# Performance work log

Hardware: AMD Instinct MI355X
Metric: run time of the kernel (lower is better)

Reference implementation:

```python
import jax, jax.numpy as jnp
import numpy as np

EPS = 1e-6
T = 8            # max_recursion_depth
STACK = 16       # stack_size
K = 1024         # n_symbols
CC = 0.25        # commitment_cost
ETH_W = 0.005    # ethical_weight
PONDER = 1e-4    # ponder_penalty
B, DIM, V = 1024, 512, 32000


def _clin(Wr, Wi, zr, zi):
    # complex linear: (Wr + i Wi)(zr + i zi), nn.Linear convention x @ W.T
    return zr @ Wr.T - zi @ Wi.T, zi @ Wr.T + zr @ Wi.T


def _cnorm(scale, shift, zr, zi):
    mag = jnp.sqrt(zr * zr + zi * zi) + EPS
    mean = mag.mean(-1, keepdims=True)
    var = mag.var(-1, keepdims=True, ddof=1)  # torch.var unbiased=True
    nm = (mag - mean) / jnp.sqrt(var + EPS) * scale + shift
    ph = jnp.arctan2(zi, zr)
    return nm * jnp.cos(ph), nm * jnp.sin(ph)


def _modrelu(b, zr, zi):
    n = jnp.sqrt(zr * zr + zi * zi) + EPS
    s = jax.nn.relu(n + b) / n
    return zr * s, zi * s


def setup_inputs() -> dict:
    key = jax.random.key(0)
    ks = jax.random.split(key, 24)
    g = lambda k, sh, s=0.02: (jax.random.normal(k, sh, jnp.float32) * s)
    xav = lambda k, sh: jax.random.uniform(k, sh, jnp.float32, -1, 1) * np.sqrt(6.0 / (sh[0] + sh[1]))
    return {
        'input_ids': jax.random.randint(ks[0], (B, 1), 0, V),
        'emb_mag': g(ks[1], (V, DIM), 1.0),
        'emb_phase': g(ks[2], (V, DIM), 1.0),
        'lin_r': xav(ks[3], (DIM, DIM)), 'lin_i': xav(ks[4], (DIM, DIM)),
        'norm_scale': jnp.ones((DIM,), jnp.float32), 'norm_shift': jnp.zeros((DIM,), jnp.float32),
        'mod_bias': jnp.zeros((DIM,), jnp.float32),
        'halt_W': g(ks[5], (1, 2 * DIM)), 'halt_b': jnp.full((1,), -2.0, jnp.float32),
        'ctrl_W': g(ks[6], (3, 2 * DIM)), 'ctrl_b': jnp.zeros((3,), jnp.float32),
        'q_r': xav(ks[7], (DIM, DIM)), 'q_i': xav(ks[8], (DIM, DIM)),
        'k_r': xav(ks[9], (DIM, DIM)), 'k_i': xav(ks[10], (DIM, DIM)),
        'v_r': xav(ks[11], (DIM, DIM)), 'v_i': xav(ks[12], (DIM, DIM)),
        'codebook': jax.random.normal(ks[13], (K, 2 * DIM), jnp.float32),
        'adjacency': jnp.zeros((K, K), jnp.float32),
        'dec_W': g(ks[14], (V, 2 * DIM)), 'dec_b': jnp.zeros((V,), jnp.float32),
    }


def reference(input_ids, emb_mag, emb_phase, lin_r, lin_i, norm_scale, norm_shift, mod_bias,
              halt_W, halt_b, ctrl_W, ctrl_b, q_r, q_i, k_r, k_i, v_r, v_i,
              codebook, adjacency, dec_W, dec_b):
    dim = emb_mag.shape[1]
    b = input_ids.shape[0]
    idx = input_ids[:, 0]
    r, th = emb_mag[idx], emb_phase[idx]
    zr, zi = r * jnp.cos(th), r * jnp.sin(th)  # [B, dim] complex embedding

    mem = jnp.zeros((b, STACK, 2 * dim), zr.dtype)
    ptr = jnp.zeros((b, STACK), zr.dtype).at[:, 0].set(1.0)
    remain = jnp.ones((b, 1), zr.dtype)
    zwr = jnp.zeros_like(zr); zwi = jnp.zeros_like(zi)
    ponder = jnp.float32(0.0); vq_tot = jnp.float32(0.0)
    eth_tot = jnp.float32(0.0); prev = None
    scale = dim ** -0.5

    for step in range(T):
        # AdaptiveRecursiveCell: linear -> norm -> modrelu -> attention
        pr, pi = _clin(lin_r, lin_i, zr, zi)
        pr, pi = _cnorm(norm_scale, norm_shift, pr, pi)
        pr, pi = _modrelu(mod_bias, pr, pi)
        qr, qi = _clin(q_r, q_i, pr, pi)
        kr, ki = _clin(k_r, k_i, pr, pi)
        vr, vi = _clin(v_r, v_i, pr, pi)
        qf = jnp.concatenate([qr, qi], -1)
        kf = jnp.concatenate([kr, ki], -1)
        A = jax.nn.softmax(qf @ kf.T * scale, -1)  # [B, B] cross-batch attention
        pr, pi = A @ vr, A @ vi
        zf = jnp.concatenate([pr, pi], -1)  # [B, 2dim]
        halt = jax.nn.sigmoid(zf @ halt_W.T + halt_b)        # [B, 1]
        ctrl = jax.nn.softmax(zf @ ctrl_W.T + ctrl_b, -1)    # [B, 3]

        # DifferentiableStack
        push, pop, noop = ctrl[:, :1], ctrl[:, 1:2], ctrl[:, 2:3]
        ptr_up = jnp.roll(ptr, 1, axis=1)
        ptr_dn = jnp.roll(ptr, -1, axis=1)
        nptr = push * ptr_up + pop * ptr_dn + noop * ptr
        nptr = nptr / (nptr.sum(1, keepdims=True) + EPS)
        wm = push * ptr_up  # [B, STACK]
        mem = wm[:, :, None] * zf[:, None, :] + mem * (1.0 - wm[:, :, None])
        read = (mem * nptr[:, :, None]).sum(1)  # [B, 2dim]
        ptr = nptr
        cr = pr + read[:, :dim]; ci = pi + read[:, dim:]

        # GraphMemoryVQ (batched path: graph bias branch is a no-op)
        cf = jnp.concatenate([cr, ci], -1)
        d = ((cf * cf).sum(-1, keepdims=True) + (codebook * codebook).sum(-1)
             - 2.0 * cf @ codebook.T)  # [B, K]
        sym = jnp.argmin(d, -1)
        zq = codebook[sym]
        vq_tot = vq_tot + jnp.mean((zq - jax.lax.stop_gradient(cf)) ** 2) \
                 + CC * jnp.mean((jax.lax.stop_gradient(zq) - cf) ** 2)
        zq = cf + jax.lax.stop_gradient(zq - cf)  # straight-through
        sr, si = zq[:, :dim], zq[:, dim:]

        # EthicalConstraint: cross_entropy(adjacency[prev], curr)
        if prev is not None:
            row = adjacency[prev]  # [B, K]
            eth = jnp.mean(jax.nn.logsumexp(row, -1)
                           - jnp.take_along_axis(row, sym[:, None], 1)[:, 0])
            eth_tot = eth_tot + eth
        prev = sym

        # ACT weighting
        w = remain if step == T - 1 else halt * remain
        zwr = zwr + w * sr; zwi = zwi + w * si
        remain = remain * (1.0 - halt)
        ponder = ponder + remain.mean()
        zr, zi = sr, si

    logits = jnp.concatenate([zwr, zwi], -1) @ dec_W.T + dec_b  # [B, V]
    aux_loss = vq_tot + ETH_W * eth_tot + PONDER * ponder
    return logits, aux_loss
```

## Files before the change

kernel.cpp:

```cpp
#include <hip/hip_runtime.h>
#include <math.h>

#define NB 1024
#define ND 512
#define ND2 1024
#define NSTEPS 8
#define NSTACK 16
#define NK 1024
#define NV 32000
#define FEPS 1e-6f
#define ATT_SCALE 0.044194173824159216f

typedef _Float16 f16;
typedef f16 f16x8 __attribute__((ext_vector_type(8)));
typedef f16 f16x4 __attribute__((ext_vector_type(4)));
typedef float f32x4 __attribute__((ext_vector_type(4)));

__device__ __forceinline__ int swz(int row, int chunk) {
    return row * 32 + ((chunk ^ ((row >> 1) & 3)) * 8);
}

__device__ __forceinline__ void gl16(const f16* g, f16* l) {
    __builtin_amdgcn_global_load_lds(
        (const __attribute__((address_space(1))) void*)g,
        (__attribute__((address_space(3))) void*)l, 16, 0, 0);
}

__device__ __forceinline__ float blk_sum(float v, float* red) {
    int t = threadIdx.x;
    red[t] = v; __syncthreads();
    for (int s = 128; s > 0; s >>= 1) {
        if (t < s) red[t] += red[t + s];
        __syncthreads();
    }
    float r = red[0]; __syncthreads();
    return r;
}

__device__ __forceinline__ float blk_max(float v, float* red) {
    int t = threadIdx.x;
    red[t] = v; __syncthreads();
    for (int s = 128; s > 0; s >>= 1) {
        if (t < s) red[t] = fmaxf(red[t], red[t + s]);
        __syncthreads();
    }
    float r = red[0]; __syncthreads();
    return r;
}

__device__ __forceinline__ void split_write(float v, f16* oh, f16* ol, size_t idx) {
    f16 h = (f16)v;
    oh[idx] = h;
    ol[idx] = (f16)((v - (float)h) * 1024.f);
}

__global__ __launch_bounds__(256)
void k_init(float* ptrb, float* remainb, float* scal) {
    int i = blockIdx.x * 256 + threadIdx.x;
    if (i < NB) {
        remainb[i] = 1.f;
        for (int s = 0; s < NSTACK; ++s) ptrb[i * NSTACK + s] = (s == 0) ? 1.f : 0.f;
    }
    if (i < 8) scal[i] = 0.f;
}

__global__ __launch_bounds__(256)
void k_embed(const int* __restrict__ ids, const float* __restrict__ mag,
             const float* __restrict__ ph, f16* __restrict__ zh, f16* __restrict__ zl) {
    int b = blockIdx.x;
    int id = ids[b];
    for (int d = threadIdx.x; d < ND; d += 256) {
        float m = mag[(size_t)id * ND + d];
        float p = ph[(size_t)id * ND + d];
        split_write(m * cosf(p), zh, zl, (size_t)b * ND2 + d);
        split_write(m * sinf(p), zh, zl, (size_t)b * ND2 + ND + d);
    }
}

__global__ __launch_bounds__(256)
void k_cbnorm(const float* __restrict__ cb, float* __restrict__ cbn) {
    __shared__ float red[256];
    int k = blockIdx.x;
    float s = 0.f;
    for (int c = threadIdx.x; c < ND2; c += 256) {
        float v = cb[(size_t)k * ND2 + c];
        s += v * v;
    }
    float tot = blk_sum(s, red);
    if (threadIdx.x == 0) cbn[k] = tot;
}

__global__ __launch_bounds__(256)
void k_lse(const float* __restrict__ adj, float* __restrict__ lse) {
    __shared__ float red[256];
    int k = blockIdx.x, t = threadIdx.x;
    float lm = -INFINITY;
    for (int c = t; c < NK; c += 256) lm = fmaxf(lm, adj[(size_t)k * NK + c]);
    float mxa = blk_max(lm, red);
    float le = 0.f;
    for (int c = t; c < NK; c += 256) le += expf(adj[(size_t)k * NK + c] - mxa);
    float se = blk_sum(le, red);
    if (t == 0) lse[k] = mxa + logf(se);
}

__global__ __launch_bounds__(256)
void k_buildW(const float* __restrict__ Wr, const float* __restrict__ Wi,
              f16* __restrict__ oh, f16* __restrict__ ol, int transp) {
    int idx = blockIdx.x * 256 + threadIdx.x;
    int n = idx >> 10, k = idx & 1023;
    int r = transp ? k : n, c = transp ? n : k;
    float v;
    if (r < 512) v = (c < 512) ? Wr[r * 512 + c] : -Wi[r * 512 + (c - 512)];
    else { int r2 = r - 512; v = (c < 512) ? Wi[r2 * 512 + c] : Wr[r2 * 512 + (c - 512)]; }
    split_write(v, oh, ol, idx);
}

__global__ __launch_bounds__(256)
void k_splitcb(const float* __restrict__ in, f16* __restrict__ oh, f16* __restrict__ ol) {
    int idx = blockIdx.x * 256 + threadIdx.x;
    split_write(in[idx], oh, ol, idx);
}

__global__ __launch_bounds__(256)
void k_split_h(const float* __restrict__ in, f16* __restrict__ oh, size_t n) {
    size_t i = (size_t)blockIdx.x * 256 + threadIdx.x;
    size_t st = (size_t)gridDim.x * 256;
    for (; i < n; i += st) oh[i] = (f16)in[i];
}

__global__ __launch_bounds__(256)
void k_split1(const float* __restrict__ in, f16* __restrict__ oh, f16* __restrict__ ol) {
    int idx = blockIdx.x * 256 + threadIdx.x;
    split_write(in[idx], oh, ol, idx);
}

template<int EPI>
__global__ __launch_bounds__(512, 4)
void k_sgemm5(const f16* __restrict__ Ah, const f16* __restrict__ Al,
              const f16* __restrict__ Bh, const f16* __restrict__ Bl,
              float* __restrict__ Cf,
              f16* __restrict__ qh, f16* __restrict__ ql,
              f16* __restrict__ vTh, f16* __restrict__ vTl,
              int N, int K, float alpha) {
    __shared__ f16 lds[2][2][4][64 * 32];
    const int tid = threadIdx.x;
    const int g = tid >> 8;
    const int gt = tid & 255;
    const int srow = gt >> 2, scb = gt & 3;
    const int soff = swz(srow, scb);
    const int lane = tid & 63;
    const int q = (tid >> 6) & 3;
    const int qr = (q >> 1) * 32, qc = (q & 1) * 32;
    const int fr = lane & 15, cbk = lane >> 4;
    const int m0 = blockIdx.y * 64, n0 = blockIdx.x * 64;
    const int kbase = g * (K >> 1);
    const int iters = K >> 6;

    const f16* pA  = Ah + (size_t)(m0 + srow) * K + kbase + scb * 8;
    const f16* pAl_ = Al + (size_t)(m0 + srow) * K + kbase + scb * 8;
    const f16* pB  = Bh + (size_t)(n0 + srow) * K + kbase + scb * 8;
    const f16* pBl_ = Bl + (size_t)(n0 + srow) * K + kbase + scb * 8;

    f32x4 z4 = {0.f, 0.f, 0.f, 0.f};
    f32x4 acc0[2][2] = {{z4, z4}, {z4, z4}};
    f32x4 acc1[2][2] = {{z4, z4}, {z4, z4}};

    f16x8 rA  = *(const f16x8*)pA;
    f16x8 rAl = *(const f16x8*)pAl_;
    f16x8 rB  = *(const f16x8*)pB;
    f16x8 rBl = *(const f16x8*)pBl_;
    *(f16x8*)&lds[0][g][0][soff] = rA;
    *(f16x8*)&lds[0][g][1][soff] = rAl;
    *(f16x8*)&lds[0][g][2][soff] = rB;
    *(f16x8*)&lds[0][g][3][soff] = rBl;
    if (iters > 1) {
        rA  = *(const f16x8*)(pA + 32);
        rAl = *(const f16x8*)(pAl_ + 32);
        rB  = *(const f16x8*)(pB + 32);
        rBl = *(const f16x8*)(pBl_ + 32);
    }
    __syncthreads();

    for (int it = 0; it < iters; ++it) {
        const int cur = it & 1;
        f16x8 ah[2], al[2], bh[2], bl[2];
        #pragma unroll
        for (int i = 0; i < 2; ++i) {
            int ra = qr + i * 16 + fr;
            int oa = swz(ra, cbk);
            ah[i] = *(const f16x8*)&lds[cur][g][0][oa];
            al[i] = *(const f16x8*)&lds[cur][g][1][oa];
            int rb = qc + i * 16 + fr;
            int ob = swz(rb, cbk);
            bh[i] = *(const f16x8*)&lds[cur][g][2][ob];
            bl[i] = *(const f16x8*)&lds[cur][g][3][ob];
        }
        if (it + 1 < iters) {
            *(f16x8*)&lds[cur ^ 1][g][0][soff] = rA;
            *(f16x8*)&lds[cur ^ 1][g][1][soff] = rAl;
            *(f16x8*)&lds[cur ^ 1][g][2][soff] = rB;
            *(f16x8*)&lds[cur ^ 1][g][3][soff] = rBl;
            if (it + 2 < iters) {
                int ko = (it + 2) * 32;
                rA  = *(const f16x8*)(pA + ko);
                rAl = *(const f16x8*)(pAl_ + ko);
                rB  = *(const f16x8*)(pB + ko);
                rBl = *(const f16x8*)(pBl_ + ko);
            }
        }
        #pragma unroll
        for (int i = 0; i < 2; ++i)
            #pragma unroll
            for (int j = 0; j < 2; ++j) {
                acc0[i][j] = __builtin_amdgcn_mfma_f32_16x16x32_f16(ah[i], bh[j], acc0[i][j], 0, 0, 0);
                acc1[i][j] = __builtin_amdgcn_mfma_f32_16x16x32_f16(ah[i], bl[j], acc1[i][j], 0, 0, 0);
                acc1[i][j] = __builtin_amdgcn_mfma_f32_16x16x32_f16(al[i], bh[j], acc1[i][j], 0, 0, 0);
            }
        __syncthreads();
    }

    float val[2][2][4];
    #pragma unroll
    for (int i = 0; i < 2; ++i)
        #pragma unroll
        for (int j = 0; j < 2; ++j)
            #pragma unroll
            for (int jj = 0; jj < 4; ++jj)
                val[i][j][jj] = acc0[i][j][jj] + acc1[i][j][jj] * 9.765625e-4f;

    float* red = (float*)&lds[0][0][0][0];
    if (g == 1) {
        #pragma unroll
        for (int i = 0; i < 2; ++i)
            #pragma unroll
            for (int j = 0; j < 2; ++j) {
                int r = i * 16 + (lane >> 4) * 4, c = j * 16 + (lane & 15);
                #pragma unroll
                for (int jj = 0; jj < 4; ++jj)
                    red[q * 1056 + (r + jj) * 33 + c] = val[i][j][jj];
            }
    }
    __syncthreads();
    if (g == 0) {
        #pragma unroll
        for (int i = 0; i < 2; ++i)
            #pragma unroll
            for (int j = 0; j < 2; ++j) {
                int r = i * 16 + (lane >> 4) * 4, c = j * 16 + (lane & 15);
                #pragma unroll
                for (int jj = 0; jj < 4; ++jj)
                    val[i][j][jj] += red[q * 1056 + (r + jj) * 33 + c];
                int orow = m0 + qr + r;
                int ocol = n0 + qc + c;
                if constexpr (EPI == 0) {
                    #pragma unroll
                    for (int jj = 0; jj < 4; ++jj)
                        Cf[(size_t)(orow + jj) * N + ocol] = alpha * val[i][j][jj];
                } else {
                    int sec = ocol >> 10, lc = ocol & 1023;
                    if (sec == 0) {
                        #pragma unroll
                        for (int jj = 0; jj < 4; ++jj)
                            split_write(val[i][j][jj], qh, ql, (size_t)(orow + jj) * ND2 + lc);
                    } else {
                        f16x4 th, tl;
                        #pragma unroll
                        for (int jj = 0; jj < 4; ++jj) {
                            float v = val[i][j][jj];
                            f16 h = (f16)v;
                            th[jj] = h;
                            tl[jj] = (f16)((v - (float)h) * 1024.f);
                        }
                        *(f16x4*)&vTh[(size_t)lc * ND2 + orow] = th;
                        *(f16x4*)&vTl[(size_t)lc * ND2 + orow] = tl;
                    }
                }
            }
    }
}

__global__ __launch_bounds__(512, 4)
void k_dgemm6(const f16* __restrict__ A, const f16* __restrict__ B,
              float* __restrict__ C, const float* __restrict__ bias) {
    __shared__ f16 sA[2][256 * 32];
    __shared__ f16 sB[2][128 * 32];
    const int bid = blockIdx.x;
    const int l2 = (bid & 7) * 125 + (bid >> 3);
    const int m0 = (l2 & 3) * 256;
    const int n0 = (l2 >> 2) * 128;
    const int tid = threadIdx.x;
    const int lane = tid & 63, w = tid >> 6;
    const int wr = (w >> 1) * 64, wc = (w & 1) * 64;
    const int fr = lane & 15, cbk = lane >> 4;
    const int K = ND2;
    const int srow = lane >> 2, pch = lane & 3;

    f32x4 z4 = {0.f, 0.f, 0.f, 0.f};
    f32x4 acc[4][4];
    #pragma unroll
    for (int i = 0; i < 4; ++i)
        #pragma unroll
        for (int j = 0; j < 4; ++j) acc[i][j] = z4;

    auto STAGE = [&](int itn, int nbuf) {
        int ko = itn * 32;
        #pragma unroll
        for (int c = 0; c < 3; ++c) {
            int m = w * 3 + c;
            if (m < 16) {
                int row = m * 16 + srow;
                int chunk = (pch ^ ((row >> 1) & 3)) * 8;
                gl16(A + (size_t)(m0 + row) * K + ko + chunk, (f16*)&sA[nbuf][m * 512]);
            } else {
                int mm = m - 16;
                int row = mm * 16 + srow;
                int chunk = (pch ^ ((row >> 1) & 3)) * 8;
                gl16(B + (size_t)(n0 + row) * K + ko + chunk, (f16*)&sB[nbuf][mm * 512]);
            }
        }
    };

    STAGE(0, 0);
    __syncthreads();

    for (int it = 0; it < 32; ++it) {
        const int cur = it & 1;
        if (it + 1 < 32) STAGE(it + 1, cur ^ 1);
        f16x8 a[4], b[4];
        #pragma unroll
        for (int i = 0; i < 4; ++i) {
            int rra = wr + i * 16 + fr;
            a[i] = *(const f16x8*)&sA[cur][swz(rra, cbk)];
        }
        #pragma unroll
        for (int j = 0; j < 4; ++j) {
            int rrb = wc + j * 16 + fr;
            b[j] = *(const f16x8*)&sB[cur][swz(rrb, cbk)];
        }
        #pragma unroll
        for (int i = 0; i < 4; ++i)
            #pragma unroll
            for (int j = 0; j < 4; ++j)
                acc[i][j] = __builtin_amdgcn_mfma_f32_16x16x32_f16(a[i], b[j], acc[i][j], 0, 0, 0);
        __syncthreads();
    }
    #pragma unroll
    for (int i = 0; i < 4; ++i)
        #pragma unroll
        for (int j = 0; j < 4; ++j) {
            int orow = m0 + wr + i * 16 + (lane >> 4) * 4;
            int ocol = n0 + wc + j * 16 + (lane & 15);
            float bv = bias[ocol];
            #pragma unroll
            for (int jj = 0; jj < 4; ++jj)
                C[(size_t)(orow + jj) * NV + ocol] = acc[i][j][jj] + bv;
        }
}

__global__ __launch_bounds__(256)
void k_cnorm(const float* __restrict__ p, const float* __restrict__ CW1,
             const int* __restrict__ sym,
             f16* __restrict__ ph, f16* __restrict__ pl,
             const float* __restrict__ scale, const float* __restrict__ shift,
             const float* __restrict__ mbias) {
    __shared__ float red[256];
    int b = blockIdx.x, t = threadIdx.x;
    const float* row = sym ? (CW1 + (size_t)sym[b] * ND2) : (p + (size_t)b * ND2);
    float xr[2], xi[2], hv[2];
    float lsum = 0.f;
    #pragma unroll
    for (int l = 0; l < 2; ++l) {
        int d = t + l * 256;
        float a = row[d], c = row[ND + d];
        xr[l] = a; xi[l] = c;
        float h = sqrtf(a * a + c * c);
        hv[l] = h;
        lsum += h + FEPS;
    }
    float mean = blk_sum(lsum, red) * (1.f / ND);
    float lvar = 0.f;
    #pragma unroll
    for (int l = 0; l < 2; ++l) {
        float dv = (hv[l] + FEPS) - mean;
        lvar += dv * dv;
    }
    float var = blk_sum(lvar, red) * (1.f / (ND - 1));
    float istd = 1.f / sqrtf(var + FEPS);
    #pragma unroll
    for (int l = 0; l < 2; ++l) {
        int d = t + l * 256;
        float nm = ((hv[l] + FEPS) - mean) * istd * scale[d] + shift[d];
        float cc, ss;
        if (hv[l] > 0.f) { cc = xr[l] / hv[l]; ss = xi[l] / hv[l]; }
        else             { cc = 1.f; ss = 0.f; }
        float vr_ = nm * cc, vi_ = nm * ss;
        float n = sqrtf(vr_ * vr_ + vi_ * vi_) + FEPS;
        float aarg = n + mbias[d];
        float sg = (aarg > 0.f ? aarg : 0.f) / n;
        split_write(vr_ * sg, ph, pl, (size_t)b * ND2 + d);
        split_write(vi_ * sg, ph, pl, (size_t)b * ND2 + ND + d);
    }
}

__global__ __launch_bounds__(256)
void k_softmax2(const float* __restrict__ SS, const int* __restrict__ sym,
                f16* __restrict__ Ah, f16* __restrict__ Al) {
    __shared__ float red[256];
    __shared__ int syms[NB];
    int row = blockIdx.x, t = threadIdx.x;
    for (int i = t; i < NB; i += 256) syms[i] = sym[i];
    __syncthreads();
    const float* Srow = SS + (size_t)syms[row] * NK;
    float v[4];
    float lm = -INFINITY;
    #pragma unroll
    for (int l = 0; l < 4; ++l) {
        v[l] = ATT_SCALE * Srow[syms[t + l * 256]];
        lm = fmaxf(lm, v[l]);
    }
    float mx = blk_max(lm, red);
    float ls = 0.f;
    #pragma unroll
    for (int l = 0; l < 4; ++l) { v[l] = expf(v[l] - mx); ls += v[l]; }
    float tot = blk_sum(ls, red);
    float inv = 1024.f / tot;
    #pragma unroll
    for (int l = 0; l < 4; ++l)
        split_write(v[l] * inv, Ah, Al, (size_t)row * NB + t + l * 256);
}

__global__ __launch_bounds__(256)
void k_gatherVT(const f16* __restrict__ VTh, const f16* __restrict__ VTl,
                const int* __restrict__ sym,
                f16* __restrict__ vTh, f16* __restrict__ vTl) {
    __shared__ int syms[NB];
    int n = blockIdx.x, t = threadIdx.x;
    for (int i = t; i < NB; i += 256) syms[i] = sym[i];
    __syncthreads();
    const f16* rh = VTh + (size_t)n * NK;
    const f16* rl = VTl + (size_t)n * NK;
    for (int b = t; b < NB; b += 256) {
        int s = syms[b];
        vTh[(size_t)n * NB + b] = rh[s];
        vTl[(size_t)n * NB + b] = rl[s];
    }
}

__global__ __launch_bounds__(256)
void k_softmax(const float* __restrict__ S, f16* __restrict__ Ah, f16* __restrict__ Al) {
    __shared__ float red[256];
    int row = blockIdx.x, t = threadIdx.x;
    float v[4];
    float lm = -INFINITY;
    #pragma unroll
    for (int l = 0; l < 4; ++l) {
        v[l] = S[(size_t)row * NB + t + l * 256];
        lm = fmaxf(lm, v[l]);
    }
    float mx = blk_max(lm, red);
    float ls = 0.f;
    #pragma unroll
    for (int l = 0; l < 4; ++l) { v[l] = expf(v[l] - mx); ls += v[l]; }
    float tot = blk_sum(ls, red);
    float inv = 1024.f / tot;
    #pragma unroll
    for (int l = 0; l < 4; ++l)
        split_write(v[l] * inv, Ah, Al, (size_t)row * NB + t + l * 256);
}

__global__ __launch_bounds__(256)
void k_stack2(const float* __restrict__ zfh, int step,
              const float* __restrict__ hW, const float* __restrict__ hB,
              const float* __restrict__ cW, const float* __restrict__ cB,
              float* __restrict__ ptrb, float* __restrict__ Ptab,
              float* __restrict__ haltb, float* __restrict__ cfn,
              f16* __restrict__ cfh, f16* __restrict__ cfl) {
    __shared__ float zfs[ND2];
    __shared__ float red[256];
    __shared__ float pt[NSTACK], npv[NSTACK], wmv[NSTACK];
    __shared__ float coef[NSTEPS];
    __shared__ float snorm;
    int b = blockIdx.x, t = threadIdx.x;
    const float* zf = zfh + (size_t)step * NB * ND2 + (size_t)b * ND2;
    for (int c = t; c < ND2; c += 256) zfs[c] = zf[c];
    __syncthreads();
    float dh = 0, d0 = 0, d1 = 0, d2 = 0;
    for (int c = t; c < ND2; c += 256) {
        float z = zfs[c];
        dh += z * hW[c];
        d0 += z * cW[c];
        d1 += z * cW[ND2 + c];
        d2 += z * cW[2 * ND2 + c];
    }
    dh = blk_sum(dh, red);
    d0 = blk_sum(d0, red);
    d1 = blk_sum(d1, red);
    d2 = blk_sum(d2, red);
    float h = 1.f / (1.f + expf(-(dh + hB[0])));
    float l0 = d0 + cB[0], l1 = d1 + cB[1], l2 = d2 + cB[2];
    float mx = fmaxf(l0, fmaxf(l1, l2));
    float e0 = expf(l0 - mx), e1 = expf(l1 - mx), e2 = expf(l2 - mx);
    float es = e0 + e1 + e2;
    float push = e0 / es, pop = e1 / es, noop = e2 / es;
    if (t < NSTACK) pt[t] = ptrb[b * NSTACK + t];
    __syncthreads();
    if (t < NSTACK) {
        float up = pt[(t + NSTACK - 1) & 15];
        float dn = pt[(t + 1) & 15];
        npv[t] = push * up + pop * dn + noop * pt[t];
        wmv[t] = push * up;
    }
    __syncthreads();
    if (t == 0) {
        float s = 0.f;
        for (int j = 0; j < NSTACK; ++j) s += npv[j];
        snorm = 1.f / (s + FEPS);
    }
    __syncthreads();
    if (t < NSTACK) {
        npv[t] *= snorm;
        ptrb[b * NSTACK + t] = npv[t];
        float om = 1.f - wmv[t];
        for (int u = 0; u < step; ++u)
            Ptab[((size_t)b * NSTEPS + u) * NSTACK + t] *= om;
        Ptab[((size_t)b * NSTEPS + step) * NSTACK + t] = wmv[t];
    }
    __syncthreads();
    if (t <= step) {
        float s = 0.f;
        #pragma unroll
        for (int j = 0; j < NSTACK; ++j)
            s += npv[j] * Ptab[((size_t)b * NSTEPS + t) * NSTACK + j];
        coef[t] = s;
    }
    __syncthreads();
    float lq = 0.f;
    for (int c = t; c < ND2; c += 256) {
        float rd = coef[step] * zfs[c];
        for (int u = 0; u < step; ++u)
            rd += coef[u] * zfh[(size_t)u * NB * ND2 + (size_t)b * ND2 + c];
        float v = zfs[c] + rd;
        split_write(v, cfh, cfl, (size_t)b * ND2 + c);
        lq += v * v;
    }
    float q = blk_sum(lq, red);
    if (t == 0) { cfn[b] = q; haltb[b] = h; }
}

__global__ __launch_bounds__(256)
void k_vqstep(const float* __restrict__ G, const float* __restrict__ cb,
              const float* __restrict__ cbn, const float* __restrict__ cfn,
              const float* __restrict__ adj, const float* __restrict__ lse,
              const float* __restrict__ haltb,
              float* __restrict__ remainb, float* __restrict__ zw,
              f16* __restrict__ zwh, f16* __restrict__ zwl,
              int* __restrict__ prev, float* __restrict__ scal,
              int step, int islast) {
    __shared__ float sval[256];
    __shared__ int sidx[256];
    int b = blockIdx.x, t = threadIdx.x;
    float bv = INFINITY; int bi = NK;
    for (int k = t; k < NK; k += 256) {
        float v = cbn[k] - 2.f * G[(size_t)b * NK + k];
        if (v < bv) { bv = v; bi = k; }
    }
    sval[t] = bv; sidx[t] = bi;
    __syncthreads();
    for (int s = 128; s > 0; s >>= 1) {
        if (t < s) {
            float ov = sval[t + s]; int oi = sidx[t + s];
            if (ov < sval[t] || (ov == sval[t] && oi < sidx[t])) { sval[t] = ov; sidx[t] = oi; }
        }
        __syncthreads();
    }
    int sym = sidx[0];
    float sdt = sval[0] + cfn[b];
    float contrib = 0.f;
    if (step > 0) {
        int pv = prev[b];
        contrib = lse[pv] - adj[(size_t)pv * NK + sym];
    }
    float hb = haltb[b];
    float rm = remainb[b];
    float w = islast ? rm : hb * rm;
    for (int c = t; c < ND2; c += 256) {
        size_t idx = (size_t)b * ND2 + c;
        float nv = zw[idx] + w * cb[(size_t)sym * ND2 + c];
        if (islast) split_write(nv, zwh, zwl, idx);
        else zw[idx] = nv;
    }
    if (t == 0) {
        float nrm = rm * (1.f - hb);
        remainb[b] = nrm;
        atomicAdd(&scal[0], sdt);
        if (step > 0) atomicAdd(&scal[1], contrib);
        atomicAdd(&scal[2], nrm);
        prev[b] = sym;
    }
}

__global__ void k_aux(const float* __restrict__ scal, float* __restrict__ out) {
    out[0] = 1.25f * scal[0] / (1024.f * 1024.f)
           + 0.005f * (scal[1] / 1024.f)
           + 0.0001f * (scal[2] / 1024.f);
}

extern "C" void kernel_launch(void* const* d_in, const int* in_sizes, int n_in,
                              void* d_out, int out_size, void* d_ws, size_t ws_size,
                              hipStream_t stream) {
    const int*   input_ids  = (const int*)  d_in[0];
    const float* emb_mag    = (const float*)d_in[1];
    const float* emb_phase  = (const float*)d_in[2];
    const float* lin_r      = (const float*)d_in[3];
    const float* lin_i      = (const float*)d_in[4];
    const float* norm_scale = (const float*)d_in[5];
    const float* norm_shift = (const float*)d_in[6];
    const float* mod_bias   = (const float*)d_in[7];
    const float* halt_W     = (const float*)d_in[8];
    const float* halt_b     = (const float*)d_in[9];
    const float* ctrl_W     = (const float*)d_in[10];
    const float* ctrl_b     = (const float*)d_in[11];
    const float* q_r        = (const float*)d_in[12];
    const float* q_i        = (const float*)d_in[13];
    const float* k_r        = (const float*)d_in[14];
    const float* k_i        = (const float*)d_in[15];
    const float* v_r        = (const float*)d_in[16];
    const float* v_i        = (const float*)d_in[17];
    const float* codebook   = (const float*)d_in[18];
    const float* adjacency  = (const float*)d_in[19];
    const float* dec_W      = (const float*)d_in[20];
    const float* dec_b      = (const float*)d_in[21];
    float* out = (float*)d_out;

    float* fb = (float*)d_ws;
    size_t o = 0;
    auto af = [&](size_t n) { float* p = fb + o; o += n; return p; };
    float* scr      = af((size_t)NB * ND2);
    float* SS       = af((size_t)NK * NK);
    float* zfh      = af((size_t)NSTEPS * NB * ND2);
    float* CW1      = af((size_t)NK * ND2);
    float* zw       = af((size_t)NB * ND2);
    float* Ptab     = af((size_t)NB * NSTEPS * NSTACK);
    float* ptrb     = af((size_t)NB * NSTACK);
    float* haltb    = af(NB);
    float* remainb  = af(NB);
    float* cbn      = af(NK);
    float* cfn      = af(NB);
    float* lse      = af(NK);
    int*   prev     = (int*)af(NB);
    float* scal     = af(8);

    f16* hbuf = (f16*)(fb + o);
    size_t ho = 0;
    auto ah = [&](size_t n) { f16* q = hbuf + ho; ho += n; return q; };
    f16* z_h   = ah((size_t)NB * ND2);
    f16* z_l   = ah((size_t)NB * ND2);
    f16* p_h   = ah((size_t)NB * ND2);
    f16* p_l   = ah((size_t)NB * ND2);
    f16* t_h   = ah((size_t)NB * ND2);
    f16* t_l   = ah((size_t)NB * ND2);
    f16* vT_h  = ah((size_t)NB * ND2);
    f16* vT_l  = ah((size_t)NB * ND2);
    f16* VTt_h = ah((size_t)ND2 * NK);
    f16* VTt_l = ah((size_t)ND2 * NK);
    f16* Pn_h  = ah((size_t)NK * ND2);
    f16* Pn_l  = ah((size_t)NK * ND2);
    f16* A_h   = ah((size_t)NB * NB);
    f16* A_l   = ah((size_t)NB * NB);
    f16* cf_h  = ah((size_t)NB * ND2);
    f16* cf_l  = ah((size_t)NB * ND2);
    f16* zw_h  = ah((size_t)NB * ND2);
    f16* zw_l  = ah((size_t)NB * ND2);
    f16* W1_h  = ah((size_t)ND2 * ND2);
    f16* W1_l  = ah((size_t)ND2 * ND2);
    f16* WqT_h = ah((size_t)ND2 * ND2);
    f16* WqT_l = ah((size_t)ND2 * ND2);
    f16* WkT_h = ah((size_t)ND2 * ND2);
    f16* WkT_l = ah((size_t)ND2 * ND2);
    f16* Bc_h  = ah((size_t)2 * ND2 * ND2);
    f16* Bc_l  = ah((size_t)2 * ND2 * ND2);
    f16* cb_h  = ah((size_t)NK * ND2);
    f16* cb_l  = ah((size_t)NK * ND2);
    f16* dW_h  = ah((size_t)NV * ND2);

    hipMemsetAsync(zw, 0, (size_t)NB * ND2 * sizeof(float), stream);
    k_init<<<4, 256, 0, stream>>>(ptrb, remainb, scal);
    k_embed<<<NB, 256, 0, stream>>>(input_ids, emb_mag, emb_phase, z_h, z_l);
    k_cbnorm<<<NK, 256, 0, stream>>>(codebook, cbn);
    k_lse<<<NK, 256, 0, stream>>>(adjacency, lse);
    k_buildW<<<(ND2 * ND2) / 256, 256, 0, stream>>>(lin_r, lin_i, W1_h, W1_l, 0);
    k_buildW<<<(ND2 * ND2) / 256, 256, 0, stream>>>(q_r, q_i, WqT_h, WqT_l, 1);
    k_buildW<<<(ND2 * ND2) / 256, 256, 0, stream>>>(k_r, k_i, WkT_h, WkT_l, 1);
    k_buildW<<<(ND2 * ND2) / 256, 256, 0, stream>>>(v_r, v_i,
        Bc_h + (size_t)ND2 * ND2, Bc_l + (size_t)ND2 * ND2, 0);
    k_splitcb<<<(NK * ND2) / 256, 256, 0, stream>>>(codebook, cb_h, cb_l);
    k_split_h<<<2048, 256, 0, stream>>>(dec_W, dW_h, (size_t)NV * ND2);
    k_sgemm5<0><<<dim3(16, 16), 512, 0, stream>>>(WkT_h, WkT_l, WqT_h, WqT_l, scr,
        nullptr, nullptr, nullptr, nullptr, ND2, ND2, 1.f);
    k_split1<<<(ND2 * ND2) / 256, 256, 0, stream>>>(scr, Bc_h, Bc_l);
    k_sgemm5<0><<<dim3(16, 16), 512, 0, stream>>>(cb_h, cb_l, W1_h, W1_l, CW1,
        nullptr, nullptr, nullptr, nullptr, ND2, ND2, 1.f);
    k_cnorm<<<NK, 256, 0, stream>>>(CW1, nullptr, nullptr, Pn_h, Pn_l,
                                    norm_scale, norm_shift, mod_bias);
    k_sgemm5<2><<<dim3(32, 16), 512, 0, stream>>>(Pn_h, Pn_l, Bc_h, Bc_l, nullptr,
        t_h, t_l, VTt_h, VTt_l, 2 * ND2, ND2, 1.f);
    k_sgemm5<0><<<dim3(16, 16), 512, 0, stream>>>(t_h, t_l, Pn_h, Pn_l, SS,
        nullptr, nullptr, nullptr, nullptr, NK, ND2, 1.f);

    for (int step = 0; step < NSTEPS; ++step) {
        if (step == 0) {
            k_sgemm5<0><<<dim3(16, 16), 512, 0, stream>>>(z_h, z_l, W1_h, W1_l, scr,
                nullptr, nullptr, nullptr, nullptr, ND2, ND2, 1.f);
            k_cnorm<<<NB, 256, 0, stream>>>(scr, nullptr, nullptr, p_h, p_l,
                                            norm_scale, norm_shift, mod_bias);
            k_sgemm5<2><<<dim3(32, 16), 512, 0, stream>>>(p_h, p_l, Bc_h, Bc_l, nullptr,
                t_h, t_l, vT_h, vT_l, 2 * ND2, ND2, 1.f);
            k_sgemm5<0><<<dim3(16, 16), 512, 0, stream>>>(t_h, t_l, p_h, p_l, scr,
                nullptr, nullptr, nullptr, nullptr, NB, ND2, ATT_SCALE);
            k_softmax<<<NB, 256, 0, stream>>>(scr, A_h, A_l);
        } else {
            k_softmax2<<<NB, 256, 0, stream>>>(SS, prev, A_h, A_l);
            k_gatherVT<<<ND2, 256, 0, stream>>>(VTt_h, VTt_l, prev, vT_h, vT_l);
        }
        k_sgemm5<0><<<dim3(16, 16), 512, 0, stream>>>(A_h, A_l, vT_h, vT_l,
            zfh + (size_t)step * NB * ND2,
            nullptr, nullptr, nullptr, nullptr, ND2, NB, 9.765625e-4f);
        k_stack2<<<NB, 256, 0, stream>>>(zfh, step, halt_W, halt_b, ctrl_W, ctrl_b,
                                         ptrb, Ptab, haltb, cfn, cf_h, cf_l);
        k_sgemm5<0><<<dim3(16, 16), 512, 0, stream>>>(cf_h, cf_l, cb_h, cb_l, scr,
            nullptr, nullptr, nullptr, nullptr, NK, ND2, 1.f);
        k_vqstep<<<NB, 256, 0, stream>>>(scr, codebook, cbn, cfn, adjacency, lse, haltb, remainb,
                                         zw, zw_h, zw_l, prev, scal, step, step == NSTEPS - 1 ? 1 : 0);
    }
    k_dgemm6<<<1000, 512, 0, stream>>>(zw_h, dW_h, out, dec_b);
    k_aux<<<1, 1, 0, stream>>>(scal, out + (size_t)NB * NV);
}
```

Before: 1.184 ms.

## Fuse VQ argmin into codebook GEMM epilogue and merge softmax/gather kernels

Measured after the change: 1.198 ms. No clear change (+1.3%).

```diff
diff --git a/kernel.cpp b/kernel.cpp
--- a/kernel.cpp
+++ b/kernel.cpp
@@ -15,6 +15,7 @@
 typedef f16 f16x8 __attribute__((ext_vector_type(8)));
 typedef f16 f16x4 __attribute__((ext_vector_type(4)));
 typedef float f32x4 __attribute__((ext_vector_type(4)));
+typedef unsigned long long u64;
 
 __device__ __forceinline__ int swz(int row, int chunk) {
     return row * 32 + ((chunk ^ ((row >> 1) & 3)) * 8);
@@ -24,6 +25,21 @@
     __builtin_amdgcn_global_load_lds(
         (const __attribute__((address_space(1))) void*)g,
         (__attribute__((address_space(3))) void*)l, 16, 0, 0);
+}
+
+__device__ __forceinline__ u64 fkey(float v, int idx) {
+    unsigned int ub = __float_as_uint(v);
+    unsigned int ord = (ub & 0x80000000u) ? ~ub : (ub | 0x80000000u);
+    return ((u64)ord << 32) | (unsigned int)idx;
+}
+
+__device__ __forceinline__ void amin_lds(u64* a, u64 k) {
+    u64 old = *a;
+    while (k < old) {
+        u64 prev = atomicCAS(a, old, k);
+        if (prev == old) break;
+        old = prev;
+    }
 }
 
 __device__ __forceinline__ float blk_sum(float v, float* red) {
@@ -55,10 +71,11 @@
 }
 
 __global__ __launch_bounds__(256)
-void k_init(float* ptrb, float* remainb, float* scal) {
+void k_init(float* ptrb, float* remainb, float* scal, u64* amin) {
     int i = blockIdx.x * 256 + threadIdx.x;
     if (i < NB) {
         remainb[i] = 1.f;
+        amin[i] = ~0ULL;
         for (int s = 0; s < NSTACK; ++s) ptrb[i * NSTACK + s] = (s == 0) ? 1.f : 0.f;
     }
     if (i < 8) scal[i] = 0.f;
@@ -141,8 +158,10 @@
               float* __restrict__ Cf,
               f16* __restrict__ qh, f16* __restrict__ ql,
               f16* __restrict__ vTh, f16* __restrict__ vTl,
-              int N, int K, float alpha) {
+              int N, int K, float alpha,
+              const float* __restrict__ cbnv, u64* __restrict__ amin) {
     __shared__ f16 lds[2][2][4][64 * 32];
+    __shared__ u64 aml[64];
     const int tid = threadIdx.x;
     const int g = tid >> 8;
     const int gt = tid & 255;
@@ -239,6 +258,9 @@
                 for (int jj = 0; jj < 4; ++jj)
                     red[q * 1056 + (r + jj) * 33 + c] = val[i][j][jj];
             }
+        if constexpr (EPI == 3) {
+            if (gt < 64) aml[gt] = ~0ULL;
+        }
     }
     __syncthreads();
     if (g == 0) {
@@ -256,7 +278,7 @@
                     #pragma unroll
                     for (int jj = 0; jj < 4; ++jj)
                         Cf[(size_t)(orow + jj) * N + ocol] = alpha * val[i][j][jj];
-                } else {
+                } else if constexpr (EPI == 2) {
                     int sec = ocol >> 10, lc = ocol & 1023;
                     if (sec == 0) {
                         #pragma unroll
@@ -274,8 +296,19 @@
                         *(f16x4*)&vTh[(size_t)lc * ND2 + orow] = th;
                         *(f16x4*)&vTl[(size_t)lc * ND2 + orow] = tl;
                     }
+                } else {
+                    float cbv = cbnv[ocol];
+                    #pragma unroll
+                    for (int jj = 0; jj < 4; ++jj) {
+                        float v = cbv - 2.f * val[i][j][jj];
+                        amin_lds(&aml[qr + r + jj], fkey(v, ocol));
+                    }
                 }
             }
+    }
+    if constexpr (EPI == 3) {
+        __syncthreads();
+        if (tid < 64) atomicMin(&amin[m0 + tid], aml[tid]);
     }
 }
 
@@ -403,46 +436,43 @@
 }
 
 __global__ __launch_bounds__(256)
-void k_softmax2(const float* __restrict__ SS, const int* __restrict__ sym,
-                f16* __restrict__ Ah, f16* __restrict__ Al) {
+void k_attprep(const float* __restrict__ SS, const int* __restrict__ sym,
+               const f16* __restrict__ VTh, const f16* __restrict__ VTl,
+               f16* __restrict__ Ah, f16* __restrict__ Al,
+               f16* __restrict__ vTh, f16* __restrict__ vTl) {
     __shared__ float red[256];
     __shared__ int syms[NB];
-    int row = blockIdx.x, t = threadIdx.x;
+    int t = threadIdx.x;
     for (int i = t; i < NB; i += 256) syms[i] = sym[i];
     __syncthreads();
-    const float* Srow = SS + (size_t)syms[row] * NK;
-    float v[4];
-    float lm = -INFINITY;
-    #pragma unroll
-    for (int l = 0; l < 4; ++l) {
-        v[l] = ATT_SCALE * Srow[syms[t + l * 256]];
-        lm = fmaxf(lm, v[l]);
-    }
-    float mx = blk_max(lm, red);
-    float ls = 0.f;
-    #pragma unroll
-    for (int l = 0; l < 4; ++l) { v[l] = expf(v[l] - mx); ls += v[l]; }
-    float tot = blk_sum(ls, red);
-    float inv = 1024.f / tot;
-    #pragma unroll
-    for (int l = 0; l < 4; ++l)
-        split_write(v[l] * inv, Ah, Al, (size_t)row * NB + t + l * 256);
-}
-
-__global__ __launch_bounds__(256)
-void k_gatherVT(const f16* __restrict__ VTh, const f16* __restrict__ VTl,
-                const int* __restrict__ sym,
-                f16* __restrict__ vTh, f16* __restrict__ vTl) {
-    __shared__ int syms[NB];
-    int n = blockIdx.x, t = threadIdx.x;
-    for (int i = t; i < NB; i += 256) syms[i] = sym[i];
-    __syncthreads();
-    const f16* rh = VTh + (size_t)n * NK;
-    const f16* rl = VTl + (size_t)n * NK;
-    for (int b = t; b < NB; b += 256) {
-        int s = syms[b];
-        vTh[(size_t)n * NB + b] = rh[s];
-        vTl[(size_t)n * NB + b] = rl[s];
+    if (blockIdx.x < NB) {
+        int row = blockIdx.x;
+        const float* Srow = SS + (size_t)syms[row] * NK;
+        float v[4];
+        float lm = -INFINITY;
+        #pragma unroll
+        for (int l = 0; l < 4; ++l) {
+            v[l] = ATT_SCALE * Srow[syms[t + l * 256]];
+            lm = fmaxf(lm, v[l]);
+        }
+        float mx = blk_max(lm, red);
+        float ls = 0.f;
+        #pragma unroll
+        for (int l = 0; l < 4; ++l) { v[l] = expf(v[l] - mx); ls += v[l]; }
+        float tot = blk_sum(ls, red);
+        float inv = 1024.f / tot;
+        #pragma unroll
+        for (int l = 0; l < 4; ++l)
+            split_write(v[l] * inv, Ah, Al, (size_t)row * NB + t + l * 256);
+    } else {
+        int n = blockIdx.x - NB;
+        const f16* rh = VTh + (size_t)n * NK;
+        const f16* rl = VTl + (size_t)n * NK;
+        for (int b = t; b < NB; b += 256) {
+            int s = syms[b];
+            vTh[(size_t)n * NB + b] = rh[s];
+            vTl[(size_t)n * NB + b] = rl[s];
+        }
     }
 }
 
@@ -548,33 +578,21 @@
 }
 
 __global__ __launch_bounds__(256)
-void k_vqstep(const float* __restrict__ G, const float* __restrict__ cb,
-              const float* __restrict__ cbn, const float* __restrict__ cfn,
-              const float* __restrict__ adj, const float* __restrict__ lse,
-              const float* __restrict__ haltb,
-              float* __restrict__ remainb, float* __restrict__ zw,
-              f16* __restrict__ zwh, f16* __restrict__ zwl,
-              int* __restrict__ prev, float* __restrict__ scal,
-              int step, int islast) {
-    __shared__ float sval[256];
-    __shared__ int sidx[256];
+void k_vqstep2(u64* __restrict__ amin, const float* __restrict__ cb,
+               const float* __restrict__ cfn,
+               const float* __restrict__ adj, const float* __restrict__ lse,
+               const float* __restrict__ haltb,
+               float* __restrict__ remainb, float* __restrict__ zw,
+               f16* __restrict__ zwh, f16* __restrict__ zwl,
+               int* __restrict__ prev, float* __restrict__ scal,
+               int step, int islast) {
     int b = blockIdx.x, t = threadIdx.x;
-    float bv = INFINITY; int bi = NK;
-    for (int k = t; k < NK; k += 256) {
-        float v = cbn[k] - 2.f * G[(size_t)b * NK + k];
-        if (v < bv) { bv = v; bi = k; }
-    }
-    sval[t] = bv; sidx[t] = bi;
-    __syncthreads();
-    for (int s = 128; s > 0; s >>= 1) {
-        if (t < s) {
-            float ov = sval[t + s]; int oi = sidx[t + s];
-            if (ov < sval[t] || (ov == sval[t] && oi < sidx[t])) { sval[t] = ov; sidx[t] = oi; }
-        }
-        __syncthreads();
-    }
-    int sym = sidx[0];
-    float sdt = sval[0] + cfn[b];
+    u64 key = amin[b];
+    int sym = (int)(key & 0xFFFFFFFFu);
+    unsigned int ord = (unsigned int)(key >> 32);
+    unsigned int ub = (ord & 0x80000000u) ? (ord & 0x7FFFFFFFu) : ~ord;
+    float sval0 = __uint_as_float(ub);
+    float sdt = sval0 + cfn[b];
     float contrib = 0.f;
     if (step > 0) {
         int pv = prev[b];
@@ -596,6 +614,7 @@
         if (step > 0) atomicAdd(&scal[1], contrib);
         atomicAdd(&scal[2], nrm);
         prev[b] = sym;
+        amin[b] = ~0ULL;
     }
 }
 
@@ -648,6 +667,7 @@
     float* cfn      = af(NB);
     float* lse      = af(NK);
     int*   prev     = (int*)af(NB);
+    u64*   amin     = (u64*)af(2 * NB);
     float* scal     = af(8);
 
     f16* hbuf = (f16*)(fb + o);
@@ -684,7 +704,7 @@
     f16* dW_h  = ah((size_t)NV * ND2);
 
     hipMemsetAsync(zw, 0, (size_t)NB * ND2 * sizeof(float), stream);
-    k_init<<<4, 256, 0, stream>>>(ptrb, remainb, scal);
+    k_init<<<4, 256, 0, stream>>>(ptrb, remainb, scal, amin);
     k_embed<<<NB, 256, 0, stream>>>(input_ids, emb_mag, emb_phase, z_h, z_l);
     k_cbnorm<<<NK, 256, 0, stream>>>(codebook, cbn);
     k_lse<<<NK, 256, 0, stream>>>(adjacency, lse);
@@ -696,41 +716,42 @@
     k_splitcb<<<(NK * ND2) / 256, 256, 0, stream>>>(codebook, cb_h, cb_l);
     k_split_h<<<2048, 256, 0, stream>>>(dec_W, dW_h, (size_t)NV * ND2);
     k_sgemm5<0><<<dim3(16, 16), 512, 0, stream>>>(WkT_h, WkT_l, WqT_h, WqT_l, scr,
-        nullptr, nullptr, nullptr, nullptr, ND2, ND2, 1.f);
+        nullptr, nullptr, nullptr, nullptr, ND2, ND2, 1.f, nullptr, nullptr);
     k_split1<<<(ND2 * ND2) / 256, 256, 0, stream>>>(scr, Bc_h, Bc_l);
     k_sgemm5<0><<<dim3(16, 16), 512, 0, stream>>>(cb_h, cb_l, W1_h, W1_l, CW1,
-        nullptr, nullptr, nullptr, nullptr, ND2, ND2, 1.f);
+        nullptr, nullptr, nullptr, nullptr, ND2, ND2, 1.f, nullptr, nullptr);
     k_cnorm<<<NK, 256, 0, stream>>>(CW1, nullptr, nullptr, Pn_h, Pn_l,
                                     norm_scale, norm_shift, mod_bias);
     k_sgemm5<2><<<dim3(32, 16), 512, 0, stream>>>(Pn_h, Pn_l, Bc_h, Bc_l, nullptr,
-        t_h, t_l, VTt_h, VTt_l, 2 * ND2, ND2, 1.f);
+        t_h, t_l, VTt_h, VTt_l, 2 * ND2, ND2, 1.f, nullptr, nullptr);
     k_sgemm5<0><<<dim3(16, 16), 512, 0, stream>>>(t_h, t_l, Pn_h, Pn_l, SS,
-        nullptr, nullptr, nullptr, nullptr, NK, ND2, 1.f);
+        nullptr, nullptr, nullptr, nullptr, NK, ND2, 1.f, nullptr, nullptr);
 
     for (int step = 0; step < NSTEPS; ++step) {
         if (step == 0) {
             k_sgemm5<0><<<dim3(16, 16), 512, 0, stream>>>(z_h, z_l, W1_h, W1_l, scr,
-                nullptr, nullptr, nullptr, nullptr, ND2, ND2, 1.f);
+                nullptr, nullptr, nullptr, nullptr, ND2, ND2, 1.f, nullptr, nullptr);
             k_cnorm<<<NB, 256, 0, stream>>>(scr, nullptr, nullptr, p_h, p_l,
                                             norm_scale, norm_shift, mod_bias);
             k_sgemm5<2><<<dim3(32, 16), 512, 0, stream>>>(p_h, p_l, Bc_h, Bc_l, nullptr,
-                t_h, t_l, vT_h, vT_l, 2 * ND2, ND2, 1.f);
+                t_h, t_l, vT_h, vT_l, 2 * ND2, ND2, 1.f, nullptr, nullptr);
             k_sgemm5<0><<<dim3(16, 16), 512, 0, stream>>>(t_h, t_l, p_h, p_l, scr,
-                nullptr, nullptr, nullptr, nullptr, NB, ND2, ATT_SCALE);
+                nullptr, nullptr, nullptr, nullptr, NB, ND2, ATT_SCALE, nullptr, nullptr);
             k_softmax<<<NB, 256, 0, stream>>>(scr, A_h, A_l);
         } else {
-            k_softmax2<<<NB, 256, 0, stream>>>(SS, prev, A_h, A_l);
-            k_gatherVT<<<ND2, 256, 0, stream>>>(VTt_h, VTt_l, prev, vT_h, vT_l);
+            k_attprep<<<2 * NB, 256, 0, stream>>>(SS, prev, VTt_h, VTt_l,
+                                                  A_h, A_l, vT_h, vT_l);
         }
         k_sgemm5<0><<<dim3(16, 16), 512, 0, stream>>>(A_h, A_l, vT_h, vT_l,
             zfh + (size_t)step * NB * ND2,
-            nullptr, nullptr, nullptr, nullptr, ND2, NB, 9.765625e-4f);
+            nullptr, nullptr, nullptr, nullptr, ND2, NB, 9.765625e-4f, nullptr, nullptr);
         k_stack2<<<NB, 256, 0, stream>>>(zfh, step, halt_W, halt_b, ctrl_W, ctrl_b,
                                          ptrb, Ptab, haltb, cfn, cf_h, cf_l);
-        k_sgemm5<0><<<dim3(16, 16), 512, 0, stream>>>(cf_h, cf_l, cb_h, cb_l, scr,
-            nullptr, nullptr, nullptr, nullptr, NK, ND2, 1.f);
-        k_vqstep<<<NB, 256, 0, stream>>>(scr, codebook, cbn, cfn, adjacency, lse, haltb, remainb,
-                                         zw, zw_h, zw_l, prev, scal, step, step == NSTEPS - 1 ? 1 : 0);
+        k_sgemm5<3><<<dim3(16, 16), 512, 0, stream>>>(cf_h, cf_l, cb_h, cb_l, nullptr,
+            nullptr, nullptr, nullptr, nullptr, NK, ND2, 1.f, cbn, amin);
+        k_vqstep2<<<NB, 256, 0, stream>>>(amin, codebook, cfn, adjacency, lse, haltb, remainb,
+                                          zw, zw_h, zw_l, prev, scal, step,
+                                          step == NSTEPS - 1 ? 1 : 0);
     }
     k_dgemm6<<<1000, 512, 0, stream>>>(zw_h, dW_h, out, dec_b);
     k_aux<<<1, 1, 0, stream>>>(scal, out + (size_t)NB * NV);
```
